# Optimization experiments

Hardware: AMD Instinct MI355X
Metric: run time of the kernel (lower is better)

## Reference

```python
import jax, jax.numpy as jnp
import numpy as np

N_OBJ, N_REL = 5000, 20000
HID, POOL, N_RELCLS, N_OBJCLS = 512, 4096, 51, 151


def setup_inputs() -> dict:
    key = jax.random.key(0)
    ks = jax.random.split(key, 8)
    s = lambda fi, fo: (2.0 / (fi + fo)) ** 0.5  # xavier-ish scale
    return {
        'edge_ctx': jax.random.normal(ks[0], (N_OBJ, HID), jnp.float32),
        'union_features': jax.random.normal(ks[1], (N_REL, POOL), jnp.float32),
        'W_pe': jax.random.normal(ks[2], (2 * HID, HID), jnp.float32) * (10.0 * (1.0 / HID) ** 0.5),
        'b_pe': jnp.zeros((2 * HID,), jnp.float32),
        'W_pc': jax.random.normal(ks[3], (POOL, 2 * HID), jnp.float32) * s(2 * HID, POOL),
        'b_pc': jnp.zeros((POOL,), jnp.float32),
        'W_cc': jax.random.normal(ks[4], (N_RELCLS, POOL), jnp.float32) * s(POOL, N_RELCLS),
        'b_cc': jnp.zeros((N_RELCLS,), jnp.float32),
        'freq_emb': jax.random.normal(ks[5], (N_OBJCLS * N_OBJCLS, N_RELCLS), jnp.float32) * 0.1,
        'obj_preds': jax.random.randint(ks[6], (N_OBJ,), 0, N_OBJCLS, jnp.int64 if jax.config.jax_enable_x64 else jnp.int32),
        'pair_idx': jax.random.randint(ks[7], (N_REL, 2), 0, N_OBJ, jnp.int64 if jax.config.jax_enable_x64 else jnp.int32),
    }


def reference(edge_ctx, union_features, W_pe, b_pe, W_pc, b_pc, W_cc, b_cc,
              freq_emb, obj_preds, pair_idx):
    # post_emb -> relu -> split into head/tail halves ([N,2,HID] view)
    edge_rep = jax.nn.relu(edge_ctx @ W_pe.T + b_pe)          # [N, 2*HID]
    head_rep, tail_rep = edge_rep[:, :HID], edge_rep[:, HID:]

    hi, ti = pair_idx[:, 0], pair_idx[:, 1]
    prod = jnp.concatenate([head_rep[hi], tail_rep[ti]], axis=-1)  # [R, 2*HID]
    prod_rep = prod @ W_pc.T + b_pc                               # [R, POOL]

    ctx_dists = (prod_rep * union_features) @ W_cc.T + b_cc      # [R, 51]

    # frequency bias: embedding lookup at head_cls * num_obj_cls + tail_cls
    pair_lbl = obj_preds[hi] * N_OBJCLS + obj_preds[ti]
    frq_dists = freq_emb[pair_lbl]                               # [R, 51]
    # dropout p=0.3 is identity in eval mode
    return ctx_dists + frq_dists
```

## Files before the change

### kernel.cpp

```cpp
#include <hip/hip_runtime.h>

typedef unsigned short u16;
typedef unsigned int u32;
typedef __attribute__((ext_vector_type(4))) float f32x4;
typedef __attribute__((ext_vector_type(8))) __bf16 bf16x8;
typedef __attribute__((ext_vector_type(8))) u16 u16x8;

__device__ __forceinline__ u16 f2bf(float x) {
  u32 u = __float_as_uint(x);
  u32 r = (u + 0x7FFFu + ((u >> 16) & 1u)) >> 16;
  return (u16)r;
}

__device__ __forceinline__ float bf2f(u16 b) {
  return __uint_as_float((u32)b << 16);
}

__device__ __forceinline__ void gl16(const void* g, void* l) {
  auto* gp = (__attribute__((address_space(1))) u32*)(g);
  auto* lp = (__attribute__((address_space(3))) u32*)(l);
  __builtin_amdgcn_global_load_lds(gp, lp, 16, 0, 0);
}

__device__ __forceinline__ f32x4 mfma16(bf16x8 a, bf16x8 b, f32x4 c) {
  return __builtin_amdgcn_mfma_f32_16x16x32_bf16(a, b, c, 0, 0, 0);
}

__device__ __forceinline__ u16x8 cvt8(const float* p) {
  float4 a = *(const float4*)p, b = *(const float4*)(p + 4);
  u16x8 v;
  v[0] = f2bf(a.x); v[1] = f2bf(a.y); v[2] = f2bf(a.z); v[3] = f2bf(a.w);
  v[4] = f2bf(b.x); v[5] = f2bf(b.y); v[6] = f2bf(b.z); v[7] = f2bf(b.w);
  return v;
}

__global__ void k_prep(const float* __restrict__ ec, const float* __restrict__ wpe,
                       const float* __restrict__ wpc, const float* __restrict__ wcc,
                       u16* __restrict__ ecb, u16* __restrict__ wpeb,
                       u16* __restrict__ wpcb, u16* __restrict__ wccb) {
  int i = blockIdx.x * 256 + threadIdx.x;
  if (i < 320000) {
    *(u16x8*)(ecb + (long)i * 8) = cvt8(ec + (long)i * 8);
  } else if (i < 385536) {
    int j = i - 320000;
    *(u16x8*)(wpeb + (long)j * 8) = cvt8(wpe + (long)j * 8);
  } else if (i < 909824) {
    int j = i - 385536;
    *(u16x8*)(wpcb + (long)j * 8) = cvt8(wpc + (long)j * 8);
  } else if (i < 942592) {
    int j = i - 909824;
    long base = (long)j * 8;
    int row = (int)(base >> 12);
    int col = (int)(base & 4095);
    u16x8 v;
    if (row < 51) {
      v = cvt8(wcc + (long)row * 4096 + col);
    } else {
#pragma unroll
      for (int k = 0; k < 8; ++k) v[k] = 0;
    }
    *(u16x8*)(wccb + base) = v;
  }
}

__device__ __forceinline__ void cstep(const char* sA, const char* sB,
                                      const int (&aOff)[4], const int (&bOff)[4],
                                      f32x4 (&acc)[4][4]) {
  bf16x8 af[4], bv[4];
#pragma unroll
  for (int mi = 0; mi < 4; ++mi) af[mi] = *(const bf16x8*)(sA + aOff[mi]);
#pragma unroll
  for (int ni = 0; ni < 4; ++ni) bv[ni] = *(const bf16x8*)(sB + bOff[ni]);
  __builtin_amdgcn_s_setprio(1);
#pragma unroll
  for (int mi = 0; mi < 4; ++mi)
#pragma unroll
    for (int ni = 0; ni < 4; ++ni)
      acc[mi][ni] = mfma16(af[mi], bv[ni], acc[mi][ni]);
  __builtin_amdgcn_s_setprio(0);
}

__device__ __forceinline__ void cstep64(const char* buf,
                                        const int (&aOff)[4][2], const int (&bOff)[4][2],
                                        f32x4 (&acc)[4][4]) {
  bf16x8 af[4][2], bv[4][2];
#pragma unroll
  for (int mi = 0; mi < 4; ++mi)
#pragma unroll
    for (int ks = 0; ks < 2; ++ks) af[mi][ks] = *(const bf16x8*)(buf + aOff[mi][ks]);
#pragma unroll
  for (int ni = 0; ni < 4; ++ni)
#pragma unroll
    for (int ks = 0; ks < 2; ++ks) bv[ni][ks] = *(const bf16x8*)(buf + bOff[ni][ks]);
  __builtin_amdgcn_s_setprio(1);
#pragma unroll
  for (int ks = 0; ks < 2; ++ks)
#pragma unroll
    for (int mi = 0; mi < 4; ++mi)
#pragma unroll
      for (int ni = 0; ni < 4; ++ni)
        acc[mi][ni] = mfma16(af[mi][ks], bv[ni][ks], acc[mi][ni]);
  __builtin_amdgcn_s_setprio(0);
}

__global__ __launch_bounds__(256, 2) void k_gemm1(const u16* __restrict__ A, const u16* __restrict__ B,
                                                  const float* __restrict__ bias, u16* __restrict__ outp) {
  __shared__ char lds[65536];
  int bx = blockIdx.x;
  int rb = bx >> 3, nb = bx & 7;
  int rowBase = rb * 128, nBase = nb * 128;
  int t = threadIdx.x, lane = t & 63, wid = t >> 6;
  int wr = wid >> 1, wc = wid & 1, lm = lane & 15, lg = lane >> 4;
  int ar0 = t >> 2, ar1 = 64 + ar0, c4 = t & 3;
  int sw0 = (c4 * 16) ^ (((ar0 >> 1) & 3) << 4);
  int sw1 = (c4 * 16) ^ (((ar1 >> 1) & 3) << 4);
  const char* aS0 = (const char*)(A + (long)min(rowBase + ar0, 4999) * 512) + sw0;
  const char* aS1 = (const char*)(A + (long)min(rowBase + ar1, 4999) * 512) + sw1;
  const char* bS0 = (const char*)(B + (long)(nBase + ar0) * 512) + sw0;
  const char* bS1 = (const char*)(B + (long)(nBase + ar1) * 512) + sw1;
  int t16 = t * 16;
  int aOff[4], bOff[4];
#pragma unroll
  for (int mi = 0; mi < 4; ++mi) { int r = wr * 64 + mi * 16 + lm; aOff[mi] = r * 64 + ((lg * 16) ^ (((r >> 1) & 3) << 4)); }
#pragma unroll
  for (int ni = 0; ni < 4; ++ni) { int r = wc * 64 + ni * 16 + lm; bOff[ni] = r * 64 + ((lg * 16) ^ (((r >> 1) & 3) << 4)); }
  f32x4 acc[4][4] = {};

#define STAGE_G(k, sb) do { \
    gl16(aS0 + (k) * 2, (sb) + t16); gl16(aS1 + (k) * 2, (sb) + 4096 + t16); \
    gl16(bS0 + (k) * 2, (sb) + 8192 + t16); gl16(bS1 + (k) * 2, (sb) + 12288 + t16); \
  } while (0)

  STAGE_G(0, lds);
  STAGE_G(32, lds + 16384);
  STAGE_G(64, lds + 32768);

  int cur = 0, stg = 3;
  for (int kt = 0; kt < 16; ++kt) {
    if (kt < 13) {
      char* sb = lds + stg * 16384;
      STAGE_G((kt + 3) * 32, sb);
    }
    if (kt < 13)       asm volatile("s_waitcnt vmcnt(12)" ::: "memory");
    else if (kt == 13) asm volatile("s_waitcnt vmcnt(8)" ::: "memory");
    else if (kt == 14) asm volatile("s_waitcnt vmcnt(4)" ::: "memory");
    else               asm volatile("s_waitcnt vmcnt(0)" ::: "memory");
    __builtin_amdgcn_s_barrier();
    char* cb = lds + cur * 16384;
    cstep(cb, cb + 8192, aOff, bOff, acc);
    __builtin_amdgcn_s_barrier();
    cur = (cur == 3) ? 0 : cur + 1;
    stg = (stg == 3) ? 0 : stg + 1;
  }
#undef STAGE_G

#pragma unroll
  for (int mi = 0; mi < 4; ++mi)
#pragma unroll
    for (int ni = 0; ni < 4; ++ni) {
      int n = nBase + wc * 64 + ni * 16 + lm;
      float bvv = bias[n];
#pragma unroll
      for (int rg = 0; rg < 4; ++rg) {
        int r = rowBase + wr * 64 + mi * 16 + lg * 4 + rg;
        if (r < 5000) {
          float v = acc[mi][ni][rg] + bvv;
          v = v > 0.f ? v : 0.f;
          outp[(long)r * 1024 + n] = f2bf(v);
        }
      }
    }
}

__global__ __launch_bounds__(256, 2) void k_gemm2(const u16* __restrict__ erep, const u16* __restrict__ wpc,
                                                  const float* __restrict__ bpc, u16* __restrict__ Hout,
                                                  u16* __restrict__ Tout) {
  __shared__ char lds[65536];
  int bx = blockIdx.x;
  int h = (bx >= 1280) ? 1 : 0;
  int rr = bx - h * 1280;
  int rb = rr >> 5, nb = rr & 31;
  int rowBase = rb * 128, nBase = nb * 128;
  u16* outp = h ? Tout : Hout;
  int t = threadIdx.x, lane = t & 63, wid = t >> 6;
  int wr = wid >> 1, wc = wid & 1, lm = lane & 15, lg = lane >> 4;
  int ar = t >> 3, c8 = t & 7;
  int srcswz = ((c8 ^ (ar & 7)) << 4);
  const char* aP[4];
  const char* bP[4];
#pragma unroll
  for (int i = 0; i < 4; ++i) {
    int Ra = min(rowBase + i * 32 + ar, 4999);
    aP[i] = (const char*)(erep + (long)Ra * 1024 + h * 512) + srcswz;
    int Rb = nBase + i * 32 + ar;
    bP[i] = (const char*)(wpc + (long)Rb * 1024 + h * 512) + srcswz;
  }
  int t16 = t * 16;
  int aOff[4][2], bOff[4][2];
#pragma unroll
  for (int mi = 0; mi < 4; ++mi)
#pragma unroll
    for (int ks = 0; ks < 2; ++ks) {
      int r = wr * 64 + mi * 16 + lm;
      aOff[mi][ks] = r * 128 + (((ks * 4 + lg) ^ (r & 7)) << 4);
    }
#pragma unroll
  for (int ni = 0; ni < 4; ++ni)
#pragma unroll
    for (int ks = 0; ks < 2; ++ks) {
      int r = wc * 64 + ni * 16 + lm;
      bOff[ni][ks] = 16384 + r * 128 + (((ks * 4 + lg) ^ (r & 7)) << 4);
    }
  f32x4 acc[4][4] = {};

#define STAGE2(kk, buf) do { \
    _Pragma("unroll") \
    for (int i = 0; i < 4; ++i) { \
      gl16(aP[i] + (kk) * 2, (buf) + i * 4096 + t16); \
      gl16(bP[i] + (kk) * 2, (buf) + 16384 + i * 4096 + t16); \
    } \
  } while (0)

  STAGE2(0, lds);
  for (int kt = 0; kt < 8; ++kt) {
    if (kt < 7) STAGE2((kt + 1) * 64, lds + (((kt + 1) & 1) ? 32768 : 0));
    if (kt < 7) asm volatile("s_waitcnt vmcnt(8)" ::: "memory");
    else        asm volatile("s_waitcnt vmcnt(0)" ::: "memory");
    __builtin_amdgcn_s_barrier();
    cstep64(lds + ((kt & 1) ? 32768 : 0), aOff, bOff, acc);
    __builtin_amdgcn_s_barrier();
  }
#undef STAGE2

#pragma unroll
  for (int mi = 0; mi < 4; ++mi)
#pragma unroll
    for (int ni = 0; ni < 4; ++ni) {
      int n = nBase + wc * 64 + ni * 16 + lm;
      float bvv = h ? 0.f : bpc[n];
#pragma unroll
      for (int rg = 0; rg < 4; ++rg) {
        int r = rowBase + wr * 64 + mi * 16 + lg * 4 + rg;
        if (r < 5000) {
          float v = acc[mi][ni][rg] + bvv;
          outp[(long)r * 4096 + n] = f2bf(v);
        }
      }
    }
}

__global__ __launch_bounds__(256) void k_final(
    const u16* __restrict__ H, const u16* __restrict__ T,
    const u16* __restrict__ wcc,
    const float* __restrict__ un,
    const float* __restrict__ bcc, const float* __restrict__ freq,
    const int* __restrict__ preds, const int* __restrict__ pidx,
    float* __restrict__ outp) {
  __shared__ char sU[32768];
  __shared__ int sLbl[128];
  int bx = blockIdx.x;
  int rb = bx >> 2, ps = bx & 3;
  int rowBase = rb * 128;
  int t = threadIdx.x, lane = t & 63, wid = t >> 6;
  int lm = lane & 15, lg = lane >> 4;
  int r16 = t >> 4, c16 = t & 15;

  if (t < 128) {
    int rG = min(rowBase + t, 19999);
    sLbl[t] = preds[pidx[2 * rG]] * 151 + preds[pidx[2 * rG + 1]];
  }

  u32 hoff[8], toff[8], uoff[8];
#pragma unroll
  for (int p = 0; p < 8; ++p) {
    int rG = min(rowBase + p * 16 + r16, 19999);
    hoff[p] = (u32)pidx[2 * rG] * 8192u + (u32)c16 * 16u;
    toff[p] = (u32)pidx[2 * rG + 1] * 8192u + (u32)c16 * 16u;
    uoff[p] = (u32)rG * 16384u + (u32)c16 * 32u;
  }
  const char* Hc = (const char*)H;
  const char* Tc = (const char*)T;
  const char* Uc = (const char*)un;
  int pc0 = ps * 1024;

  u16x8 ph[8], pt[8];
#pragma unroll
  for (int p = 0; p < 8; ++p) {
    ph[p] = *(const u16x8*)(Hc + hoff[p] + pc0 * 2);
    pt[p] = *(const u16x8*)(Tc + toff[p] + pc0 * 2);
  }

  f32x4 outAcc[2][4] = {};

  for (int chk = 0; chk < 8; ++chk) {
    int pcBase = pc0 + chk * 128;
#pragma unroll
    for (int p = 0; p < 8; ++p) {
      int r = p * 16 + r16;
      float4 u0 = *(const float4*)(Uc + uoff[p] + (u32)pcBase * 4u);
      float4 u1 = *(const float4*)(Uc + uoff[p] + (u32)pcBase * 4u + 16u);
      float uu[8];
      *(float4*)(uu) = u0;
      *(float4*)(uu + 4) = u1;
      u16x8 pv;
#pragma unroll
      for (int j = 0; j < 8; ++j)
        pv[j] = f2bf((bf2f(ph[p][j]) + bf2f(pt[p][j])) * uu[j]);
      *(u16x8*)(sU + r * 256 + ((c16 * 16) ^ ((r & 7) << 4))) = pv;
      if (chk < 7) {
        ph[p] = *(const u16x8*)(Hc + hoff[p] + (u32)(pcBase + 128) * 2u);
        pt[p] = *(const u16x8*)(Tc + toff[p] + (u32)(pcBase + 128) * 2u);
      }
    }
    asm volatile("s_waitcnt lgkmcnt(0)" ::: "memory");
    __builtin_amdgcn_s_barrier();

#pragma unroll
    for (int kb = 0; kb < 4; ++kb) {
      bf16x8 aU[2], bW[4];
#pragma unroll
      for (int m2 = 0; m2 < 2; ++m2) {
        int r = wid * 32 + m2 * 16 + lm;
        aU[m2] = *(const bf16x8*)(sU + r * 256 + ((kb * 64 + lg * 16) ^ ((r & 7) << 4)));
      }
#pragma unroll
      for (int ni = 0; ni < 4; ++ni)
        bW[ni] = *(const bf16x8*)(wcc + (long)(ni * 16 + lm) * 4096 + pcBase + kb * 32 + lg * 8);
      __builtin_amdgcn_s_setprio(1);
#pragma unroll
      for (int m2 = 0; m2 < 2; ++m2)
#pragma unroll
        for (int ni = 0; ni < 4; ++ni)
          outAcc[m2][ni] = mfma16(aU[m2], bW[ni], outAcc[m2][ni]);
      __builtin_amdgcn_s_setprio(0);
    }
    asm volatile("s_waitcnt lgkmcnt(0)" ::: "memory");
    __builtin_amdgcn_s_barrier();
  }

#pragma unroll
  for (int m2 = 0; m2 < 2; ++m2)
#pragma unroll
    for (int rg = 0; rg < 4; ++rg) {
      int r = wid * 32 + m2 * 16 + lg * 4 + rg;
      int rG = rowBase + r;
      if (rG < 20000) {
#pragma unroll
        for (int ni = 0; ni < 4; ++ni) {
          int c = ni * 16 + lm;
          if (c < 51) {
            float v = outAcc[m2][ni][rg];
            if (ps == 0) v += bcc[c] + freq[(long)sLbl[r] * 51 + c];
            atomicAdd(&outp[(long)rG * 51 + c], v);
          }
        }
      }
    }
}

extern "C" void kernel_launch(void* const* d_in, const int* in_sizes, int n_in,
                              void* d_out, int out_size, void* d_ws, size_t ws_size,
                              hipStream_t stream) {
  const float* edge_ctx = (const float*)d_in[0];
  const float* unionf   = (const float*)d_in[1];
  const float* W_pe     = (const float*)d_in[2];
  const float* b_pe     = (const float*)d_in[3];
  const float* W_pc     = (const float*)d_in[4];
  const float* b_pc     = (const float*)d_in[5];
  const float* W_cc     = (const float*)d_in[6];
  const float* b_cc     = (const float*)d_in[7];
  const float* freq     = (const float*)d_in[8];
  const int*   preds    = (const int*)d_in[9];
  const int*   pidx     = (const int*)d_in[10];
  float* out = (float*)d_out;
  char* ws = (char*)d_ws;

  u16* Hb   = (u16*)(ws + 0);
  u16* Tb   = (u16*)(ws + 40960000);
  u16* erep = (u16*)(ws + 81920000);
  u16* wpcb = (u16*)(ws + 92160000);
  u16* wccb = (u16*)(ws + 100548608);
  u16* ecb  = (u16*)(ws + 101072896);
  u16* wpeb = (u16*)(ws + 106192896);

  hipMemsetAsync(d_out, 0, (size_t)out_size * 4, stream);
  k_prep<<<3682, 256, 0, stream>>>(edge_ctx, W_pe, W_pc, W_cc, ecb, wpeb, wpcb, wccb);
  k_gemm1<<<320, 256, 0, stream>>>(ecb, wpeb, b_pe, erep);
  k_gemm2<<<2560, 256, 0, stream>>>(erep, wpcb, b_pc, Hb, Tb);
  k_final<<<628, 256, 0, stream>>>(Hb, Tb, wccb, unionf, b_cc, freq, preds, pidx, out);
}
```

Before: 305.3 us.

## Make each wave own its 32 rows in k_final, dropping block barriers

The staging of the H/T/union product into shared memory is remapped so each wave writes only the 32 rows its own MFMAs later read. Each lane handles one row and half of the 128-column chunk. This lets the two per-chunk block-wide barriers be replaced by a single wave-local lgkmcnt wait, with one __syncthreads before the epilogue. It also drops the cross-chunk register prefetch of H/T, and adds a launch-bounds occupancy hint of 3 blocks per CU. The new per-lane access pattern is less coalesced across lanes (each lane reads a different row), and without the prefetch, load latency must be hidden by wave interleaving and occupancy.

```diff
diff --git a/kernel.cpp b/kernel.cpp
--- a/kernel.cpp
+++ b/kernel.cpp
@@ -249,7 +249,7 @@
     }
 }
 
-__global__ __launch_bounds__(256) void k_final(
+__global__ __launch_bounds__(256, 3) void k_final(
     const u16* __restrict__ H, const u16* __restrict__ T,
     const u16* __restrict__ wcc,
     const float* __restrict__ un,
@@ -263,65 +263,60 @@
   int rowBase = rb * 128;
   int t = threadIdx.x, lane = t & 63, wid = t >> 6;
   int lm = lane & 15, lg = lane >> 4;
-  int r16 = t >> 4, c16 = t & 15;
 
   if (t < 128) {
     int rG = min(rowBase + t, 19999);
     sLbl[t] = preds[pidx[2 * rG]] * 151 + preds[pidx[2 * rG + 1]];
   }
 
-  u32 hoff[8], toff[8], uoff[8];
-#pragma unroll
-  for (int p = 0; p < 8; ++p) {
-    int rG = min(rowBase + p * 16 + r16, 19999);
-    hoff[p] = (u32)pidx[2 * rG] * 8192u + (u32)c16 * 16u;
-    toff[p] = (u32)pidx[2 * rG + 1] * 8192u + (u32)c16 * 16u;
-    uoff[p] = (u32)rG * 16384u + (u32)c16 * 32u;
-  }
-  const char* Hc = (const char*)H;
-  const char* Tc = (const char*)T;
-  const char* Uc = (const char*)un;
+  int row2 = lane & 31;
+  int half = lane >> 5;
+  int r = wid * 32 + row2;
+  int rG = min(rowBase + r, 19999);
+  const u16* hp = H + (long)pidx[2 * rG] * 4096 + half * 64;
+  const u16* tp = T + (long)pidx[2 * rG + 1] * 4096 + half * 64;
+  const float* up = un + (long)rG * 4096 + half * 64;
+  char* sUr = sU + r * 256;
+  int rsw = (r & 7) << 4;
   int pc0 = ps * 1024;
-
-  u16x8 ph[8], pt[8];
-#pragma unroll
-  for (int p = 0; p < 8; ++p) {
-    ph[p] = *(const u16x8*)(Hc + hoff[p] + pc0 * 2);
-    pt[p] = *(const u16x8*)(Tc + toff[p] + pc0 * 2);
-  }
 
   f32x4 outAcc[2][4] = {};
 
   for (int chk = 0; chk < 8; ++chk) {
     int pcBase = pc0 + chk * 128;
 #pragma unroll
-    for (int p = 0; p < 8; ++p) {
-      int r = p * 16 + r16;
-      float4 u0 = *(const float4*)(Uc + uoff[p] + (u32)pcBase * 4u);
-      float4 u1 = *(const float4*)(Uc + uoff[p] + (u32)pcBase * 4u + 16u);
-      float uu[8];
-      *(float4*)(uu) = u0;
-      *(float4*)(uu + 4) = u1;
-      u16x8 pv;
-#pragma unroll
-      for (int j = 0; j < 8; ++j)
-        pv[j] = f2bf((bf2f(ph[p][j]) + bf2f(pt[p][j])) * uu[j]);
-      *(u16x8*)(sU + r * 256 + ((c16 * 16) ^ ((r & 7) << 4))) = pv;
-      if (chk < 7) {
-        ph[p] = *(const u16x8*)(Hc + hoff[p] + (u32)(pcBase + 128) * 2u);
-        pt[p] = *(const u16x8*)(Tc + toff[p] + (u32)(pcBase + 128) * 2u);
+    for (int qq = 0; qq < 2; ++qq) {
+      int c0 = pcBase + qq * 32;
+      u16x8 h8[4], t8[4];
+#pragma unroll
+      for (int i = 0; i < 4; ++i) {
+        h8[i] = *(const u16x8*)(hp + c0 + i * 8);
+        t8[i] = *(const u16x8*)(tp + c0 + i * 8);
+      }
+#pragma unroll
+      for (int i = 0; i < 4; ++i) {
+        float4 ua = *(const float4*)(up + c0 + i * 8);
+        float4 ub = *(const float4*)(up + c0 + i * 8 + 4);
+        float uu[8];
+        *(float4*)(uu) = ua;
+        *(float4*)(uu + 4) = ub;
+        u16x8 pv;
+#pragma unroll
+        for (int j = 0; j < 8; ++j)
+          pv[j] = f2bf((bf2f(h8[i][j]) + bf2f(t8[i][j])) * uu[j]);
+        int cb = half * 128 + qq * 64 + i * 16;
+        *(u16x8*)(sUr + (cb ^ rsw)) = pv;
       }
     }
     asm volatile("s_waitcnt lgkmcnt(0)" ::: "memory");
-    __builtin_amdgcn_s_barrier();
 
 #pragma unroll
     for (int kb = 0; kb < 4; ++kb) {
       bf16x8 aU[2], bW[4];
 #pragma unroll
       for (int m2 = 0; m2 < 2; ++m2) {
-        int r = wid * 32 + m2 * 16 + lm;
-        aU[m2] = *(const bf16x8*)(sU + r * 256 + ((kb * 64 + lg * 16) ^ ((r & 7) << 4)));
+        int rr2 = wid * 32 + m2 * 16 + lm;
+        aU[m2] = *(const bf16x8*)(sU + rr2 * 256 + ((kb * 64 + lg * 16) ^ ((rr2 & 7) << 4)));
       }
 #pragma unroll
       for (int ni = 0; ni < 4; ++ni)
@@ -334,24 +329,24 @@
           outAcc[m2][ni] = mfma16(aU[m2], bW[ni], outAcc[m2][ni]);
       __builtin_amdgcn_s_setprio(0);
     }
-    asm volatile("s_waitcnt lgkmcnt(0)" ::: "memory");
-    __builtin_amdgcn_s_barrier();
-  }
+  }
+
+  __syncthreads();
 
 #pragma unroll
   for (int m2 = 0; m2 < 2; ++m2)
 #pragma unroll
     for (int rg = 0; rg < 4; ++rg) {
-      int r = wid * 32 + m2 * 16 + lg * 4 + rg;
-      int rG = rowBase + r;
-      if (rG < 20000) {
+      int rr2 = wid * 32 + m2 * 16 + lg * 4 + rg;
+      int rGo = rowBase + rr2;
+      if (rGo < 20000) {
 #pragma unroll
         for (int ni = 0; ni < 4; ++ni) {
           int c = ni * 16 + lm;
           if (c < 51) {
             float v = outAcc[m2][ni][rg];
-            if (ps == 0) v += bcc[c] + freq[(long)sLbl[r] * 51 + c];
-            atomicAdd(&outp[(long)rG * 51 + c], v);
+            if (ps == 0) v += bcc[c] + freq[(long)sLbl[rr2] * 51 + c];
+            atomicAdd(&outp[(long)rGo * 51 + c], v);
           }
         }
       }
```

New measurement: 336.3 us. 1.1x slower.
